# Kernel optimization log

Hardware: AMD Instinct MI355X
Metric: run time of the kernel (lower is better)

Reference implementation:

```python
import jax, jax.numpy as jnp
import numpy as np

B, L, D = 16, 2048, 192  # batch, frames_per_data, units
H, K = 4, 12             # num_heads, key_dim (hardcoded in build())
EPS = 1e-3               # keras LayerNormalization default epsilon


def layer_norm(x, g, b):
    m = jnp.mean(x, axis=-1, keepdims=True)
    v = jnp.mean(jnp.square(x - m), axis=-1, keepdims=True)
    return (x - m) * jax.lax.rsqrt(v + EPS) * g + b


def conv1d_valid(x, w, b):
    # x: [B,L,C], w: [3,Cin,Cout] -> [B,L-2,Cout]
    return jax.lax.conv_general_dilated(
        x, w, window_strides=(1,), padding='VALID',
        dimension_numbers=('NWC', 'WIO', 'NWC')) + b


def setup_inputs() -> dict:
    key = jax.random.key(0)
    ks = jax.random.split(key, 16)
    s = 0.05
    return {
        'x': jax.random.normal(ks[0], (B, L, D), jnp.float32),
        'ln1_g': jnp.ones((D,), jnp.float32),
        'ln1_b': jnp.zeros((D,), jnp.float32),
        'wq': jax.random.normal(ks[1], (D, H, K), jnp.float32) * s,
        'bq': jnp.zeros((H, K), jnp.float32),
        'wk': jax.random.normal(ks[2], (D, H, K), jnp.float32) * s,
        'bk': jnp.zeros((H, K), jnp.float32),
        'wv': jax.random.normal(ks[3], (D, H, K), jnp.float32) * s,
        'bv': jnp.zeros((H, K), jnp.float32),
        'wo': jax.random.normal(ks[4], (H, K, D), jnp.float32) * s,
        'bo': jnp.zeros((D,), jnp.float32),
        'ln2_g': jnp.ones((D,), jnp.float32),
        'ln2_b': jnp.zeros((D,), jnp.float32),
        'c1_w': jax.random.normal(ks[5], (3, D, D), jnp.float32) * s,
        'c1_b': jnp.zeros((D,), jnp.float32),
        'c2_w': jax.random.normal(ks[6], (3, D, D), jnp.float32) * s,
        'c2_b': jnp.zeros((D,), jnp.float32),
    }


def reference(x, ln1_g, ln1_b, wq, bq, wk, bk, wv, bv, wo, bo,
              ln2_g, ln2_b, c1_w, c1_b, c2_w, c2_b):
    # --- LN1 + causal MHA + residual (dropout = identity at inference) ---
    xn = layer_norm(x, ln1_g, ln1_b)
    q = jnp.einsum('bld,dhk->blhk', xn, wq) + bq
    k = jnp.einsum('bld,dhk->blhk', xn, wk) + bk
    v = jnp.einsum('bld,dhk->blhk', xn, wv) + bv
    scores = jnp.einsum('blhk,bmhk->bhlm', q, k) / jnp.sqrt(jnp.float32(K))
    causal = jnp.tril(jnp.ones((L, L), jnp.float32))  # tril(True) mask
    scores = scores + (1.0 - causal) * (-1e9)          # keras additive mask
    attn = jax.nn.softmax(scores, axis=-1)
    ctx = jnp.einsum('bhlm,bmhk->blhk', attn, v)
    mha = jnp.einsum('blhk,hkd->bld', ctx, wo) + bo
    x = x + mha
    # --- LN2 + positionwise Conv1D feedforward + residual ---
    xn = layer_norm(x, ln2_g, ln2_b)
    h = jax.nn.relu(conv1d_valid(xn, c1_w, c1_b))      # [B,L-2,D]
    h = jnp.pad(h, ((0, 0), (1, 1), (0, 0)))           # ZeroPadding1D(1,1)
    h = conv1d_valid(h, c2_w, c2_b)                    # [B,L-2,D]
    h = jnp.pad(h, ((0, 0), (1, 1), (0, 0)))
    return x + h
```

## Files before the change

### kernel.cpp

```cpp
#include <hip/hip_runtime.h>
#include <hip/hip_bf16.h>

#define L_ 2048
#define D_ 192
#define HK_ 48
#define EPS_ 1e-3f
#define SCALE_ 0.28867513459481287f
#define LOG2E_ 1.4426950408889634f

typedef __hip_bfloat16 bf16;
typedef _Float16 f16;
typedef __fp16 hf16x2 __attribute__((ext_vector_type(2)));
typedef _Float16 f16x4 __attribute__((ext_vector_type(4)));
typedef __bf16 bf16x4 __attribute__((ext_vector_type(4)));
typedef __bf16 bf16x8 __attribute__((ext_vector_type(8)));
typedef float  f32x4  __attribute__((ext_vector_type(4)));

__device__ __forceinline__ float b2f(bf16 x) { return __bfloat162float(x); }
__device__ __forceinline__ bf16 f2b(float x) { return __float2bfloat16(x); }

__global__ __launch_bounds__(256) void k_prep_all(
    const float* __restrict__ c1w, const float* __restrict__ c2w,
    const float* __restrict__ wq, const float* __restrict__ wk, const float* __restrict__ wv,
    const float* __restrict__ bq, const float* __restrict__ bk, const float* __restrict__ bv,
    const float* __restrict__ wo,
    bf16* __restrict__ wrep1, bf16* __restrict__ wrep2,
    bf16* __restrict__ wrepq, float* __restrict__ bias144, bf16* __restrict__ wrepo)
{
    const int i = blockIdx.x * 256 + threadIdx.x;
    if (i < 110592) {
        const int k = i / 192, n = i - k * 192;
        wrep1[((size_t)(k >> 5) * 192 + n) * 32 + (k & 31)] = f2b(c1w[i]);
    } else if (i < 221184) {
        const int j = i - 110592;
        const int k = j / 192, n = j - k * 192;
        wrep2[((size_t)(k >> 5) * 192 + n) * 32 + (k & 31)] = f2b(c2w[j]);
    } else if (i < 248832) {
        const int j = i - 221184;
        const int kb = j / 4608, rem = j % 4608;
        const int n = rem / 32, kk = rem % 32;
        const int k = kb * 32 + kk;
        float v;
        if (n < 48)       v = wq[k * HK_ + n] * (SCALE_ * LOG2E_);
        else if (n < 96)  v = wk[k * HK_ + (n - 48)];
        else              v = wv[k * HK_ + (n - 96)];
        wrepq[j] = f2b(v);
    } else if (i < 248976) {
        const int j = i - 248832;
        bias144[j] = (j < 48) ? bq[j] * (SCALE_ * LOG2E_)
                   : (j < 96) ? bk[j - 48] : bv[j - 96];
    } else if (i < 261264) {
        const int j = i - 248976;
        const int kb = j / 6144, rem = j % 6144;
        const int n = rem / 32, kk = rem % 32;
        const int k = kb * 32 + kk;
        wrepo[j] = f2b(k < 48 ? wo[k * D_ + n] : 0.f);
    }
}

__global__ __launch_bounds__(256, 4) void k_ln_qkv(
    const float* __restrict__ x, const float* __restrict__ g1, const float* __restrict__ b1,
    const bf16* __restrict__ wrep, const float* __restrict__ bias144,
    f16* __restrict__ qo, f16* __restrict__ ko, f16* __restrict__ vt)
{
    __shared__ bf16 xn[32 * 200];
    const int tid = threadIdx.x;
    const int wave = tid >> 6, lane = tid & 63;
    const int rowbase = blockIdx.x * 32;
    const int b = rowbase >> 11;
    const int lrow0 = rowbase & 2047;

    const float gg0 = g1[lane], gg1 = g1[lane + 64], gg2 = g1[lane + 128];
    const float bb0 = b1[lane], bb1 = b1[lane + 64], bb2 = b1[lane + 128];
    for (int i = 0; i < 8; ++i) {
        const int r = wave * 8 + i;
        const float* xp = x + (size_t)(rowbase + r) * D_;
        const float x0 = xp[lane];
        const float x1 = xp[lane + 64];
        const float x2 = xp[lane + 128];
        float s = x0 + x1 + x2;
        float q = x0 * x0 + x1 * x1 + x2 * x2;
        #pragma unroll
        for (int m = 1; m < 64; m <<= 1) {
            s += __shfl_xor(s, m, 64);
            q += __shfl_xor(q, m, 64);
        }
        const float mean = s * (1.0f / 192.0f);
        const float var  = q * (1.0f / 192.0f) - mean * mean;
        const float rs   = rsqrtf(var + EPS_);
        xn[r * 200 + lane]       = f2b((x0 - mean) * rs * gg0 + bb0);
        xn[r * 200 + lane + 64]  = f2b((x1 - mean) * rs * gg1 + bb1);
        xn[r * 200 + lane + 128] = f2b((x2 - mean) * rs * gg2 + bb2);
    }

    if (tid < 128) {
        const int h  = tid >> 5;
        const int vc = 12 + ((tid >> 3) & 3);
        const int p0 = lrow0 + (tid & 7) * 4;
        f16x4 vv;
        vv[0] = vv[1] = vv[2] = vv[3] = (vc == 12) ? (f16)1.0f : (f16)0.0f;
        *(f16x4*)(vt + ((size_t)(b * 4 + h) * 16 + vc) * 2048 + p0) = vv;
    }
    __syncthreads();

    const int l15 = lane & 15, q4 = lane >> 4;
    const int rt = wave >> 1, g = wave & 1;
    const int ntlim = 5 - g;
    f32x4 acc[5];
    #pragma unroll
    for (int nt = 0; nt < 5; ++nt) acc[nt] = (f32x4){0.f, 0.f, 0.f, 0.f};

    const bf16* xrow = xn + (rt * 16 + l15) * 200 + q4 * 8;
    #pragma unroll
    for (int kb = 0; kb < 6; ++kb) {
        const bf16x8 a = *(const bf16x8*)(xrow + kb * 32);
        const bf16* wp = wrep + ((size_t)kb * 144 + l15) * 32 + q4 * 8
                       + (size_t)(g * 5) * 16 * 32;
        #pragma unroll
        for (int nt = 0; nt < 5; ++nt) {
            if (nt < ntlim) {
                const bf16x8 bfr = *(const bf16x8*)(wp + (size_t)nt * 16 * 32);
                acc[nt] = __builtin_amdgcn_mfma_f32_16x16x32_bf16(a, bfr, acc[nt], 0, 0, 0);
            }
        }
    }

    const int lr0 = lrow0 + rt * 16 + q4 * 4;
    #pragma unroll
    for (int nt = 0; nt < 5; ++nt) {
        if (nt < ntlim) {
            const int ntg = g * 5 + nt;
            const int col = ntg * 16 + l15;
            const float bd = bias144[col];
            if (ntg < 3) {
                const int h2 = col / 12, c12 = col - h2 * 12;
                #pragma unroll
                for (int reg = 0; reg < 4; ++reg)
                    qo[((size_t)(b * 4 + h2) * 2048 + lr0 + reg) * 12 + c12] =
                        (f16)(acc[nt][reg] + bd);
            } else if (ntg < 6) {
                const int ck = col - 48;
                const int h2 = ck / 12, c12 = ck - h2 * 12;
                #pragma unroll
                for (int reg = 0; reg < 4; ++reg)
                    ko[((size_t)(b * 4 + h2) * 2048 + lr0 + reg) * 12 + c12] =
                        (f16)(acc[nt][reg] + bd);
            } else {
                const int vcol = col - 96;
                const int h = vcol / 12, c12 = vcol % 12;
                f16x4 vv;
                #pragma unroll
                for (int reg = 0; reg < 4; ++reg) vv[reg] = (f16)(acc[nt][reg] + bd);
                *(f16x4*)(vt + ((size_t)(b * 4 + h) * 16 + c12) * 2048 +
                          lrow0 + rt * 16 + q4 * 4) = vv;
            }
        }
    }
}

__global__ __launch_bounds__(256, 8) void k_attn_part(
    const f16* __restrict__ qh, const f16* __restrict__ kh, const f16* __restrict__ vt,
    bf16* __restrict__ part_o, float* __restrict__ part_l)
{
    const int tid = threadIdx.x;
    const int wv = tid >> 6, lane = tid & 63;
    const int quad = lane >> 4, l15 = lane & 15;
    const int bh = blockIdx.x / 36;
    int r = blockIdx.x % 36;
    int qt = 0;
    while (r >= qt + 1) { r -= qt + 1; ++qt; }
    const int ks = r;
    const size_t base  = (size_t)bh * 2048 * 12;
    const size_t vbase = ((size_t)bh * 16 + l15) * 2048;
    const int kbase = ks * 256;
    const int qbase = qt * 256 + wv * 64;
    const bool diag = (ks == qt);
    const int ktmax = diag ? 4 * (wv + 1) : 16;

    f16x4 Qf[4];
    #pragma unroll
    for (int s = 0; s < 4; ++s) {
        f16x4 v;
        if (quad < 3)
            v = *(const f16x4*)(qh + base + (size_t)(qbase + s * 16 + l15) * 12 + quad * 4);
        else { v[0] = (f16)LOG2E_; v[1] = 0; v[2] = 0; v[3] = 0; }
        Qf[s] = v;
    }

    f32x4 O[4];
    #pragma unroll
    for (int s = 0; s < 4; ++s) O[s] = (f32x4){0.f, 0.f, 0.f, 0.f};

    for (int g = 0; g < ktmax; g += 2) {
        f16x4 Kg[2], Vg[2];
        #pragma unroll
        for (int u = 0; u < 2; ++u) {
            const int kt = g + u;
            f16x4 kf;
            if (quad < 3)
                kf = *(const f16x4*)(kh + base + (size_t)(kbase + kt * 16 + l15) * 12 + quad * 4);
            else { kf[0] = (f16)-6.0f; kf[1] = 0; kf[2] = 0; kf[3] = 0; }
            Kg[u] = kf;
            Vg[u] = *(const f16x4*)(vt + vbase + kbase + kt * 16 + quad * 4);
        }
        #pragma unroll
        for (int u = 0; u < 2; ++u) {
            const int k0 = kbase + (g + u) * 16 + quad * 4;
            #pragma unroll
            for (int s = 0; s < 4; ++s) {
                f32x4 sc = (f32x4){0.f, 0.f, 0.f, 0.f};
                sc = __builtin_amdgcn_mfma_f32_16x16x16f16(Kg[u], Qf[s], sc, 0, 0, 0);
                float p0 = __builtin_amdgcn_exp2f(sc[0]);
                float p1 = __builtin_amdgcn_exp2f(sc[1]);
                float p2 = __builtin_amdgcn_exp2f(sc[2]);
                float p3 = __builtin_amdgcn_exp2f(sc[3]);
                if (diag) {
                    const int qg = qbase + s * 16 + l15;
                    p0 = (k0 + 0 <= qg) ? p0 : 0.f;
                    p1 = (k0 + 1 <= qg) ? p1 : 0.f;
                    p2 = (k0 + 2 <= qg) ? p2 : 0.f;
                    p3 = (k0 + 3 <= qg) ? p3 : 0.f;
                }
                const hf16x2 lo = __builtin_amdgcn_cvt_pkrtz(p0, p1);
                const hf16x2 hi = __builtin_amdgcn_cvt_pkrtz(p2, p3);
                f16x4 p;
                p[0] = (f16)lo[0]; p[1] = (f16)lo[1];
                p[2] = (f16)hi[0]; p[3] = (f16)hi[1];
                O[s] = __builtin_amdgcn_mfma_f32_16x16x16f16(p, Vg[u], O[s], 0, 0, 0);
            }
        }
    }

    const size_t pobase = (size_t)(bh * 8 + ks) * 2048;
    #pragma unroll
    for (int s = 0; s < 4; ++s) {
        const int q16 = qbase + s * 16;
        #pragma unroll
        for (int j = 0; j < 4; ++j) {
            const int qq = q16 + quad * 4 + j;
            if (l15 < 12)       part_o[(pobase + qq) * 12 + l15] = f2b(O[s][j]);
            else if (l15 == 12) part_l[pobase + qq] = O[s][j];
        }
    }
}

__global__ __launch_bounds__(256, 4) void k_proj_ln2(
    const float* __restrict__ x, const bf16* __restrict__ part_o,
    const float* __restrict__ part_l, const bf16* __restrict__ wrepo,
    const float* __restrict__ bo, const float* __restrict__ g2,
    const float* __restrict__ lb2, bf16* __restrict__ x2b,
    bf16* __restrict__ xn2b)
{
    __shared__ bf16 ct[32 * 72];
    __shared__ float linv[128];
    __shared__ float psum[4][4][4][2];
    const int tid = threadIdx.x;
    const int wave = tid >> 6, lane = tid & 63;
    const int rowbase = blockIdx.x * 32;
    const int b = rowbase >> 11, lrow = rowbase & 2047;
    const int ns = (lrow >> 8) + 1;

    {
        const int sub = tid >> 7, pair = tid & 127;
        const int rr = pair >> 2, h = pair & 3;
        const size_t sb = (size_t)(b * 4 + h) * 8 * 2048 + lrow + rr;
        float o[8] = {0.f, 0.f, 0.f, 0.f, 0.f, 0.f, 0.f, 0.f};
        float l = 0.f;
        if (sub == 0) {
            #pragma unroll
            for (int s = 0; s < 8; ++s) {
                if (s < ns) {
                    const bf16x8 v = *(const bf16x8*)(part_o + (sb + (size_t)s * 2048) * 12);
                    #pragma unroll
                    for (int i = 0; i < 8; ++i) o[i] += (float)v[i];
                }
            }
        } else {
            #pragma unroll
            for (int s = 0; s < 8; ++s) {
                if (s < ns) {
                    l += part_l[sb + (size_t)s * 2048];
                    const bf16x4 v = *(const bf16x4*)(part_o + (sb + (size_t)s * 2048) * 12 + 8);
                    #pragma unroll
                    for (int i = 0; i < 4; ++i) o[i] += (float)v[i];
                }
            }
            linv[pair] = 1.0f / l;
        }
        __syncthreads();
        const float inv = linv[pair];
        if (sub == 0) {
            bf16x4 w0, w1;
            #pragma unroll
            for (int i = 0; i < 4; ++i) {
                w0[i] = (__bf16)(o[i] * inv);
                w1[i] = (__bf16)(o[4 + i] * inv);
            }
            *(bf16x4*)(ct + rr * 72 + h * 12)     = w0;
            *(bf16x4*)(ct + rr * 72 + h * 12 + 4) = w1;
        } else {
            bf16x4 w, z;
            #pragma unroll
            for (int i = 0; i < 4; ++i) {
                w[i] = (__bf16)(o[i] * inv);
                z[i] = (__bf16)0.0f;
            }
            *(bf16x4*)(ct + rr * 72 + h * 12 + 8)  = w;
            *(bf16x4*)(ct + rr * 72 + 48 + h * 4)  = z;
        }
    }
    __syncthreads();

    const int l15 = lane & 15, q4 = lane >> 4;
    const int rt = wave >> 1, g = wave & 1;
    f32x4 acc[6];
    #pragma unroll
    for (int j = 0; j < 6; ++j) acc[j] = (f32x4){0.f, 0.f, 0.f, 0.f};
    const bf16* arow = ct + (rt * 16 + l15) * 72 + q4 * 8;
    #pragma unroll
    for (int kb = 0; kb < 2; ++kb) {
        const bf16x8 a = *(const bf16x8*)(arow + kb * 32);
        const bf16* wp = wrepo + ((size_t)kb * 192 + l15) * 32 + q4 * 8
                       + (size_t)(g * 6) * 16 * 32;
        #pragma unroll
        for (int j = 0; j < 6; ++j) {
            const bf16x8 bb = *(const bf16x8*)(wp + (size_t)j * 16 * 32);
            acc[j] = __builtin_amdgcn_mfma_f32_16x16x32_bf16(a, bb, acc[j], 0, 0, 0);
        }
    }

    const int rw0 = rowbase + rt * 16 + q4 * 4;
    float sum[4] = {0.f, 0.f, 0.f, 0.f}, ssum[4] = {0.f, 0.f, 0.f, 0.f};
    #pragma unroll
    for (int j = 0; j < 6; ++j) {
        const int col = (g * 6 + j) * 16 + l15;
        const float bod = bo[col];
        #pragma unroll
        for (int reg = 0; reg < 4; ++reg) {
            const float v = acc[j][reg] + bod + x[(size_t)(rw0 + reg) * D_ + col];
            acc[j][reg] = v;
            x2b[(size_t)(rw0 + reg) * D_ + col] = f2b(v);
            sum[reg] += v; ssum[reg] += v * v;
        }
    }
    #pragma unroll
    for (int m = 1; m <= 8; m <<= 1) {
        #pragma unroll
        for (int reg = 0; reg < 4; ++reg) {
            sum[reg]  += __shfl_xor(sum[reg], m, 64);
            ssum[reg] += __shfl_xor(ssum[reg], m, 64);
        }
    }
    if (l15 == 0) {
        #pragma unroll
        for (int reg = 0; reg < 4; ++reg) {
            psum[wave][q4][reg][0] = sum[reg];
            psum[wave][q4][reg][1] = ssum[reg];
        }
    }
    __syncthreads();
    float mean[4], rs[4];
    #pragma unroll
    for (int reg = 0; reg < 4; ++reg) {
        const float st = sum[reg]  + psum[wave ^ 1][q4][reg][0];
        const float qt2 = ssum[reg] + psum[wave ^ 1][q4][reg][1];
        mean[reg] = st * (1.0f / 192.0f);
        const float var = qt2 * (1.0f / 192.0f) - mean[reg] * mean[reg];
        rs[reg] = rsqrtf(var + EPS_);
    }
    #pragma unroll
    for (int j = 0; j < 6; ++j) {
        const int col = (g * 6 + j) * 16 + l15;
        const float gg = g2[col], bb2 = lb2[col];
        #pragma unroll
        for (int reg = 0; reg < 4; ++reg)
            xn2b[(size_t)(rw0 + reg) * D_ + col] =
                f2b((acc[j][reg] - mean[reg]) * rs[reg] * gg + bb2);
    }
}

#define INROWB 400
#define NIN    36
#define NH     34
#define HTOFF  (NIN * INROWB)
__global__ __launch_bounds__(256, 4) void k_conv_fused(
    const bf16* __restrict__ act, const bf16* __restrict__ w1,
    const float* __restrict__ b1c, const bf16* __restrict__ w2,
    const float* __restrict__ b2c, const bf16* __restrict__ x2b,
    float* __restrict__ outf)
{
    __shared__ __align__(16) char lds[NIN * INROWB + NH * INROWB];

    const int tid = threadIdx.x;
    const int wave = tid >> 6, lane = tid & 63;
    const int m16 = lane & 15, q = lane >> 4;
    const int rowbase = blockIdx.x * 32;
    const int lrow = rowbase & (L_ - 1);

    {
        const bf16* src0 = act + ((long long)rowbase - 2) * D_;
        bf16x8 v[4];
        int dst[4];
        #pragma unroll
        for (int i = 0; i < 4; ++i) {
            const int g = tid + i * 256;
            if (g < 864) {
                v[i] = *(const bf16x8*)(src0 + g * 8);
                const int row = (g * 2731) >> 16;
                dst[i] = row * INROWB + (g - row * 24) * 16;
            }
        }
        #pragma unroll
        for (int i = 0; i < 4; ++i) {
            const int g = tid + i * 256;
            if (g < 864) *(bf16x8*)(lds + dst[i]) = v[i];
        }
    }

    const int laneA = m16 * INROWB + q * 16;
    const int colw = wave * 48;
    float bd1[3], bd2[3];
    #pragma unroll
    for (int j = 0; j < 3; ++j) {
        bd1[j] = b1c[colw + j * 16 + m16];
        bd2[j] = b2c[colw + j * 16 + m16];
    }
    __syncthreads();

    f32x4 acc1[3][3];
    #pragma unroll
    for (int mt = 0; mt < 3; ++mt)
        #pragma unroll
        for (int j = 0; j < 3; ++j) acc1[mt][j] = (f32x4){0.f, 0.f, 0.f, 0.f};

    #define LOADB(w, kb, j) \
        (*(const bf16x8*)((w) + ((size_t)(kb) * 192 + m16) * 32 + q * 8 \
                          + (size_t)(wave * 3 + (j)) * 16 * 32))
    {
        bf16x8 bB[2][3];
        #pragma unroll
        for (int j = 0; j < 3; ++j) bB[0][j] = LOADB(w1, 0, j);
        #pragma unroll
        for (int kb = 0; kb < 18; ++kb) {
            if (kb + 1 < 18) {
                #pragma unroll
                for (int j = 0; j < 3; ++j) bB[(kb + 1) & 1][j] = LOADB(w1, kb + 1, j);
            }
            const int t = kb / 6, c6 = kb % 6;
            bf16x8 a[3];
            #pragma unroll
            for (int mt = 0; mt < 3; ++mt)
                a[mt] = *(const bf16x8*)(lds + laneA + (mt * 16 + t) * INROWB + c6 * 64);
            #pragma unroll
            for (int j = 0; j < 3; ++j)
                #pragma unroll
                for (int mt = 0; mt < 3; ++mt)
                    acc1[mt][j] = __builtin_amdgcn_mfma_f32_16x16x32_bf16(
                        a[mt], bB[kb & 1][j], acc1[mt][j], 0, 0, 0);
        }
    }

    #pragma unroll
    for (int mt = 0; mt < 3; ++mt)
        #pragma unroll
        for (int j = 0; j < 3; ++j)
            #pragma unroll
            for (int reg = 0; reg < 4; ++reg) {
                const int hr = mt * 16 + q * 4 + reg;
                if (hr < NH) {
                    const int hm = lrow + hr - 1;
                    float v = fmaxf(acc1[mt][j][reg] + bd1[j], 0.f);
                    if (hm == 0 || hm == L_ - 1) v = 0.f;
                    *(bf16*)(lds + HTOFF + hr * INROWB + (colw + j * 16 + m16) * 2) = f2b(v);
                }
            }

    float xr[3][2][4];
    #pragma unroll
    for (int j = 0; j < 3; ++j)
        #pragma unroll
        for (int mt = 0; mt < 2; ++mt)
            #pragma unroll
            for (int reg = 0; reg < 4; ++reg)
                xr[j][mt][reg] = b2f(x2b[(size_t)(rowbase + mt * 16 + q * 4 + reg) * D_
                                         + colw + j * 16 + m16]);
    __syncthreads();

    f32x4 acc2[2][3];
    #pragma unroll
    for (int mt = 0; mt < 2; ++mt)
        #pragma unroll
        for (int j = 0; j < 3; ++j) acc2[mt][j] = (f32x4){0.f, 0.f, 0.f, 0.f};
    {
        bf16x8 bB[2][3];
        #pragma unroll
        for (int j = 0; j < 3; ++j) bB[0][j] = LOADB(w2, 0, j);
        #pragma unroll
        for (int kb = 0; kb < 18; ++kb) {
            if (kb + 1 < 18) {
                #pragma unroll
                for (int j = 0; j < 3; ++j) bB[(kb + 1) & 1][j] = LOADB(w2, kb + 1, j);
            }
            const int t = kb / 6, c6 = kb % 6;
            bf16x8 a[2];
            #pragma unroll
            for (int mt = 0; mt < 2; ++mt)
                a[mt] = *(const bf16x8*)(lds + HTOFF + laneA + (mt * 16 + t) * INROWB + c6 * 64);
            #pragma unroll
            for (int j = 0; j < 3; ++j)
                #pragma unroll
                for (int mt = 0; mt < 2; ++mt)
                    acc2[mt][j] = __builtin_amdgcn_mfma_f32_16x16x32_bf16(
                        a[mt], bB[kb & 1][j], acc2[mt][j], 0, 0, 0);
        }
    }
    #undef LOADB

    #pragma unroll
    for (int j = 0; j < 3; ++j)
        #pragma unroll
        for (int mt = 0; mt < 2; ++mt)
            #pragma unroll
            for (int reg = 0; reg < 4; ++reg) {
                const int r = rowbase + mt * 16 + q * 4 + reg;
                const int m = r & (L_ - 1);
                float v = xr[j][mt][reg];
                if (m != 0 && m != L_ - 1) v += acc2[mt][j][reg] + bd2[j];
                outf[(size_t)r * D_ + colw + j * 16 + m16] = v;
            }
}

extern "C" void kernel_launch(void* const* d_in, const int* in_sizes, int n_in,
                              void* d_out, int out_size, void* d_ws, size_t ws_size,
                              hipStream_t stream)
{
    const float* x    = (const float*)d_in[0];
    const float* ln1g = (const float*)d_in[1];
    const float* ln1b = (const float*)d_in[2];
    const float* wq   = (const float*)d_in[3];
    const float* bq   = (const float*)d_in[4];
    const float* wk   = (const float*)d_in[5];
    const float* bk   = (const float*)d_in[6];
    const float* wv   = (const float*)d_in[7];
    const float* bv   = (const float*)d_in[8];
    const float* wo   = (const float*)d_in[9];
    const float* bo   = (const float*)d_in[10];
    const float* ln2g = (const float*)d_in[11];
    const float* ln2b = (const float*)d_in[12];
    const float* c1w  = (const float*)d_in[13];
    const float* c1b  = (const float*)d_in[14];
    const float* c2w  = (const float*)d_in[15];
    const float* c2b  = (const float*)d_in[16];

    const size_t ROWS = (size_t)16 * L_;
    char* ws = (char*)d_ws;
    size_t off = 4096;
    bf16* xn2b = (bf16*)(ws + off); off += ROWS * D_ * 2;
    off += 4096;
    bf16* hpb  = (bf16*)(ws + off); off += ROWS * D_ * 2;
    off += 4096;
    bf16* x2b  = (bf16*)(ws + off); off += ROWS * D_ * 2;
    f16* qb    = (f16*)(ws + off);   off += ROWS * HK_ * 2;
    f16* kb    = (f16*)(ws + off);   off += ROWS * HK_ * 2;
    f16* vt    = (f16*)(ws + off);   off += (size_t)64 * 16 * 2048 * 2;
    bf16* part_o = (bf16*)(ws + off); off += (size_t)64 * 8 * 2048 * 12 * 2;
    float* part_l = (float*)(ws + off); off += (size_t)64 * 8 * 2048 * 4;
    bf16* wrep1 = (bf16*)(ws + off); off += 576 * 192 * 2;
    bf16* wrep2 = (bf16*)(ws + off); off += 576 * 192 * 2;
    bf16* wrepq = (bf16*)(ws + off); off += 6 * 144 * 32 * 2;
    float* bias144 = (float*)(ws + off); off += 144 * 4;
    bf16* wrepo = (bf16*)(ws + off); off += 2 * 192 * 32 * 2;

    (void)hpb;
    k_prep_all   <<<1021, 256, 0, stream>>>(c1w, c2w, wq, wk, wv, bq, bk, bv, wo,
                                            wrep1, wrep2, wrepq, bias144, wrepo);
    k_ln_qkv     <<<1024, 256, 0, stream>>>(x, ln1g, ln1b, wrepq, bias144, qb, kb, vt);
    k_attn_part  <<<64 * 36, 256, 0, stream>>>(qb, kb, vt, part_o, part_l);
    k_proj_ln2   <<<1024, 256, 0, stream>>>(x, part_o, part_l, wrepo, bo, ln2g, ln2b,
                                            x2b, xn2b);
    k_conv_fused <<<1024, 256, 0, stream>>>(xn2b, wrep1, c1b, wrep2, c2b, x2b,
                                            (float*)d_out);
}
```

Baseline: 195.3 us.

## Fuse attention merge, output projection, LN2 and conv FFN into one kernel

```diff
diff --git a/kernel.cpp b/kernel.cpp
--- a/kernel.cpp
+++ b/kernel.cpp
@@ -244,189 +244,182 @@
     }
 }
 
-__global__ __launch_bounds__(256, 4) void k_proj_ln2(
+#define CIROWB 400
+#define R2OFF  14400
+#define X2OFF  28000
+#define PSOFF  40288
+__global__ __launch_bounds__(256, 3) void k_mega(
     const float* __restrict__ x, const bf16* __restrict__ part_o,
     const float* __restrict__ part_l, const bf16* __restrict__ wrepo,
     const float* __restrict__ bo, const float* __restrict__ g2,
-    const float* __restrict__ lb2, bf16* __restrict__ x2b,
-    bf16* __restrict__ xn2b)
+    const float* __restrict__ lb2, const bf16* __restrict__ w1,
+    const float* __restrict__ b1c, const bf16* __restrict__ w2,
+    const float* __restrict__ b2c, float* __restrict__ outf)
 {
-    __shared__ bf16 ct[32 * 72];
-    __shared__ float linv[128];
-    __shared__ float psum[4][4][4][2];
-    const int tid = threadIdx.x;
-    const int wave = tid >> 6, lane = tid & 63;
-    const int rowbase = blockIdx.x * 32;
-    const int b = rowbase >> 11, lrow = rowbase & 2047;
-    const int ns = (lrow >> 8) + 1;
-
-    {
-        const int sub = tid >> 7, pair = tid & 127;
-        const int rr = pair >> 2, h = pair & 3;
-        const size_t sb = (size_t)(b * 4 + h) * 8 * 2048 + lrow + rr;
-        float o[8] = {0.f, 0.f, 0.f, 0.f, 0.f, 0.f, 0.f, 0.f};
-        float l = 0.f;
-        if (sub == 0) {
-            #pragma unroll
-            for (int s = 0; s < 8; ++s) {
-                if (s < ns) {
-                    const bf16x8 v = *(const bf16x8*)(part_o + (sb + (size_t)s * 2048) * 12);
-                    #pragma unroll
-                    for (int i = 0; i < 8; ++i) o[i] += (float)v[i];
-                }
-            }
-        } else {
-            #pragma unroll
-            for (int s = 0; s < 8; ++s) {
-                if (s < ns) {
-                    l += part_l[sb + (size_t)s * 2048];
-                    const bf16x4 v = *(const bf16x4*)(part_o + (sb + (size_t)s * 2048) * 12 + 8);
-                    #pragma unroll
-                    for (int i = 0; i < 4; ++i) o[i] += (float)v[i];
-                }
-            }
-            linv[pair] = 1.0f / l;
-        }
-        __syncthreads();
-        const float inv = linv[pair];
-        if (sub == 0) {
-            bf16x4 w0, w1;
-            #pragma unroll
-            for (int i = 0; i < 4; ++i) {
-                w0[i] = (__bf16)(o[i] * inv);
-                w1[i] = (__bf16)(o[4 + i] * inv);
-            }
-            *(bf16x4*)(ct + rr * 72 + h * 12)     = w0;
-            *(bf16x4*)(ct + rr * 72 + h * 12 + 4) = w1;
-        } else {
-            bf16x4 w, z;
-            #pragma unroll
-            for (int i = 0; i < 4; ++i) {
-                w[i] = (__bf16)(o[i] * inv);
-                z[i] = (__bf16)0.0f;
-            }
-            *(bf16x4*)(ct + rr * 72 + h * 12 + 8)  = w;
-            *(bf16x4*)(ct + rr * 72 + 48 + h * 4)  = z;
-        }
-    }
-    __syncthreads();
-
-    const int l15 = lane & 15, q4 = lane >> 4;
-    const int rt = wave >> 1, g = wave & 1;
-    f32x4 acc[6];
-    #pragma unroll
-    for (int j = 0; j < 6; ++j) acc[j] = (f32x4){0.f, 0.f, 0.f, 0.f};
-    const bf16* arow = ct + (rt * 16 + l15) * 72 + q4 * 8;
-    #pragma unroll
-    for (int kb = 0; kb < 2; ++kb) {
-        const bf16x8 a = *(const bf16x8*)(arow + kb * 32);
-        const bf16* wp = wrepo + ((size_t)kb * 192 + l15) * 32 + q4 * 8
-                       + (size_t)(g * 6) * 16 * 32;
-        #pragma unroll
-        for (int j = 0; j < 6; ++j) {
-            const bf16x8 bb = *(const bf16x8*)(wp + (size_t)j * 16 * 32);
-            acc[j] = __builtin_amdgcn_mfma_f32_16x16x32_bf16(a, bb, acc[j], 0, 0, 0);
-        }
-    }
-
-    const int rw0 = rowbase + rt * 16 + q4 * 4;
-    float sum[4] = {0.f, 0.f, 0.f, 0.f}, ssum[4] = {0.f, 0.f, 0.f, 0.f};
-    #pragma unroll
-    for (int j = 0; j < 6; ++j) {
-        const int col = (g * 6 + j) * 16 + l15;
-        const float bod = bo[col];
-        #pragma unroll
-        for (int reg = 0; reg < 4; ++reg) {
-            const float v = acc[j][reg] + bod + x[(size_t)(rw0 + reg) * D_ + col];
-            acc[j][reg] = v;
-            x2b[(size_t)(rw0 + reg) * D_ + col] = f2b(v);
-            sum[reg] += v; ssum[reg] += v * v;
-        }
-    }
-    #pragma unroll
-    for (int m = 1; m <= 8; m <<= 1) {
-        #pragma unroll
-        for (int reg = 0; reg < 4; ++reg) {
-            sum[reg]  += __shfl_xor(sum[reg], m, 64);
-            ssum[reg] += __shfl_xor(ssum[reg], m, 64);
-        }
-    }
-    if (l15 == 0) {
-        #pragma unroll
-        for (int reg = 0; reg < 4; ++reg) {
-            psum[wave][q4][reg][0] = sum[reg];
-            psum[wave][q4][reg][1] = ssum[reg];
-        }
-    }
-    __syncthreads();
-    float mean[4], rs[4];
-    #pragma unroll
-    for (int reg = 0; reg < 4; ++reg) {
-        const float st = sum[reg]  + psum[wave ^ 1][q4][reg][0];
-        const float qt2 = ssum[reg] + psum[wave ^ 1][q4][reg][1];
-        mean[reg] = st * (1.0f / 192.0f);
-        const float var = qt2 * (1.0f / 192.0f) - mean[reg] * mean[reg];
-        rs[reg] = rsqrtf(var + EPS_);
-    }
-    #pragma unroll
-    for (int j = 0; j < 6; ++j) {
-        const int col = (g * 6 + j) * 16 + l15;
-        const float gg = g2[col], bb2 = lb2[col];
-        #pragma unroll
-        for (int reg = 0; reg < 4; ++reg)
-            xn2b[(size_t)(rw0 + reg) * D_ + col] =
-                f2b((acc[j][reg] - mean[reg]) * rs[reg] * gg + bb2);
-    }
-}
-
-#define INROWB 400
-#define NIN    36
-#define NH     34
-#define HTOFF  (NIN * INROWB)
-__global__ __launch_bounds__(256, 4) void k_conv_fused(
-    const bf16* __restrict__ act, const bf16* __restrict__ w1,
-    const float* __restrict__ b1c, const bf16* __restrict__ w2,
-    const float* __restrict__ b2c, const bf16* __restrict__ x2b,
-    float* __restrict__ outf)
-{
-    __shared__ __align__(16) char lds[NIN * INROWB + NH * INROWB];
+    __shared__ __align__(16) char lds[41824];
+    bf16* ct = (bf16*)(lds + R2OFF);
 
     const int tid = threadIdx.x;
     const int wave = tid >> 6, lane = tid & 63;
     const int m16 = lane & 15, q = lane >> 4;
     const int rowbase = blockIdx.x * 32;
-    const int lrow = rowbase & (L_ - 1);
-
+    const int b = rowbase >> 11, lrow = rowbase & 2047;
+    const int colw = wave * 48;
+
+    if (tid < 144) {
+        const int rr = tid >> 2, h = tid & 3;
+        int qrow = lrow + rr - 2;
+        qrow = qrow < 0 ? 0 : (qrow > 2047 ? 2047 : qrow);
+        const int nsq = (qrow >> 8) + 1;
+        const size_t sb = (size_t)(b * 4 + h) * 8 * 2048 + qrow;
+        float o[12];
+        #pragma unroll
+        for (int i = 0; i < 12; ++i) o[i] = 0.f;
+        float l = 0.f;
+        for (int s = 0; s < nsq; ++s) {
+            l += part_l[sb + (size_t)s * 2048];
+            const bf16x8 v8 = *(const bf16x8*)(part_o + (sb + (size_t)s * 2048) * 12);
+            const bf16x4 v4 = *(const bf16x4*)(part_o + (sb + (size_t)s * 2048) * 12 + 8);
+            #pragma unroll
+            for (int i = 0; i < 8; ++i) o[i] += (float)v8[i];
+            #pragma unroll
+            for (int i = 0; i < 4; ++i) o[8 + i] += (float)v4[i];
+        }
+        const float inv = 1.0f / l;
+        bf16* ctp = ct + rr * 72 + h * 12;
+        #pragma unroll
+        for (int i = 0; i < 12; ++i) ctp[i] = f2b(o[i] * inv);
+        bf16x4 z;
+        #pragma unroll
+        for (int i = 0; i < 4; ++i) z[i] = (__bf16)0.0f;
+        *(bf16x4*)(ct + rr * 72 + 48 + h * 4) = z;
+    } else {
+        const int idx = tid - 144;
+        if (idx < 108) {
+            bf16x8 z;
+            #pragma unroll
+            for (int i = 0; i < 8; ++i) z[i] = (__bf16)0.0f;
+            *(bf16x8*)(ct + 36 * 72 + idx * 8) = z;
+        }
+    }
+    float bd1[3], bd2[3], gg2[3], bbl2[3], bod[3];
+    #pragma unroll
+    for (int j = 0; j < 3; ++j) {
+        const int col = colw + j * 16 + m16;
+        bd1[j] = b1c[col]; bd2[j] = b2c[col];
+        gg2[j] = g2[col];  bbl2[j] = lb2[col]; bod[j] = bo[col];
+    }
+    __syncthreads();
+
+    f32x4 pv[3][3];
+    #pragma unroll
+    for (int mt = 0; mt < 3; ++mt)
+        #pragma unroll
+        for (int j = 0; j < 3; ++j) pv[mt][j] = (f32x4){0.f, 0.f, 0.f, 0.f};
+    #pragma unroll
+    for (int kb = 0; kb < 2; ++kb) {
+        bf16x8 a[3];
+        #pragma unroll
+        for (int mt = 0; mt < 3; ++mt)
+            a[mt] = *(const bf16x8*)(ct + (mt * 16 + m16) * 72 + kb * 32 + q * 8);
+        #pragma unroll
+        for (int j = 0; j < 3; ++j) {
+            const bf16x8 bb = *(const bf16x8*)(wrepo +
+                ((size_t)kb * 192 + (size_t)(wave * 3 + j) * 16 + m16) * 32 + q * 8);
+            #pragma unroll
+            for (int mt = 0; mt < 3; ++mt)
+                pv[mt][j] = __builtin_amdgcn_mfma_f32_16x16x32_bf16(a[mt], bb, pv[mt][j], 0, 0, 0);
+        }
+    }
+
+    #pragma unroll
+    for (int mt = 0; mt < 3; ++mt) {
+        const bool live = (mt < 2) || (q == 0);
+        #pragma unroll
+        for (int j = 0; j < 3; ++j) {
+            const int col = colw + j * 16 + m16;
+            #pragma unroll
+            for (int reg = 0; reg < 4; ++reg) {
+                int grow = lrow + mt * 16 + q * 4 + reg - 2;
+                grow = grow < 0 ? 0 : (grow > 2047 ? 2047 : grow);
+                float v = 0.f;
+                if (live)
+                    v = pv[mt][j][reg] + bod[j] + x[((size_t)b * 2048 + grow) * D_ + col];
+                pv[mt][j][reg] = v;
+            }
+        }
+    }
     {
-        const bf16* src0 = act + ((long long)rowbase - 2) * D_;
-        bf16x8 v[4];
-        int dst[4];
-        #pragma unroll
-        for (int i = 0; i < 4; ++i) {
-            const int g = tid + i * 256;
-            if (g < 864) {
-                v[i] = *(const bf16x8*)(src0 + g * 8);
-                const int row = (g * 2731) >> 16;
-                dst[i] = row * INROWB + (g - row * 24) * 16;
-            }
-        }
-        #pragma unroll
-        for (int i = 0; i < 4; ++i) {
-            const int g = tid + i * 256;
-            if (g < 864) *(bf16x8*)(lds + dst[i]) = v[i];
-        }
-    }
-
-    const int laneA = m16 * INROWB + q * 16;
-    const int colw = wave * 48;
-    float bd1[3], bd2[3];
-    #pragma unroll
-    for (int j = 0; j < 3; ++j) {
-        bd1[j] = b1c[colw + j * 16 + m16];
-        bd2[j] = b2c[colw + j * 16 + m16];
+        float* ps = (float*)(lds + PSOFF);
+        #pragma unroll
+        for (int mt = 0; mt < 3; ++mt) {
+            float sum[4], ssq[4];
+            #pragma unroll
+            for (int reg = 0; reg < 4; ++reg) {
+                sum[reg] = pv[mt][0][reg] + pv[mt][1][reg] + pv[mt][2][reg];
+                ssq[reg] = pv[mt][0][reg] * pv[mt][0][reg]
+                         + pv[mt][1][reg] * pv[mt][1][reg]
+                         + pv[mt][2][reg] * pv[mt][2][reg];
+            }
+            #pragma unroll
+            for (int m = 1; m <= 8; m <<= 1) {
+                #pragma unroll
+                for (int reg = 0; reg < 4; ++reg) {
+                    sum[reg] += __shfl_xor(sum[reg], m, 64);
+                    ssq[reg] += __shfl_xor(ssq[reg], m, 64);
+                }
+            }
+            if (m16 == 0) {
+                #pragma unroll
+                for (int reg = 0; reg < 4; ++reg) {
+                    const int tr = mt * 16 + q * 4 + reg;
+                    ps[(wave * 48 + tr) * 2 + 0] = sum[reg];
+                    ps[(wave * 48 + tr) * 2 + 1] = ssq[reg];
+                }
+            }
+        }
     }
     __syncthreads();
 
+    {
+        const float* ps = (const float*)(lds + PSOFF);
+        #pragma unroll
+        for (int mt = 0; mt < 3; ++mt) {
+            const bool live = (mt < 2) || (q == 0);
+            float mean[4], rs[4];
+            #pragma unroll
+            for (int reg = 0; reg < 4; ++reg) {
+                const int tr = mt * 16 + q * 4 + reg;
+                float st = 0.f, sq = 0.f;
+                #pragma unroll
+                for (int w = 0; w < 4; ++w) {
+                    st += ps[(w * 48 + tr) * 2 + 0];
+                    sq += ps[(w * 48 + tr) * 2 + 1];
+                }
+                mean[reg] = st * (1.0f / 192.0f);
+                const float var = sq * (1.0f / 192.0f) - mean[reg] * mean[reg];
+                rs[reg] = rsqrtf(var + EPS_);
+            }
+            if (live) {
+                #pragma unroll
+                for (int j = 0; j < 3; ++j) {
+                    const int col = colw + j * 16 + m16;
+                    #pragma unroll
+                    for (int reg = 0; reg < 4; ++reg) {
+                        const int tr = mt * 16 + q * 4 + reg;
+                        const float v = pv[mt][j][reg];
+                        const float xn = (v - mean[reg]) * rs[reg] * gg2[j] + bbl2[j];
+                        *(bf16*)(lds + tr * CIROWB + col * 2) = f2b(xn);
+                        if (tr >= 2 && tr < 34)
+                            *(bf16*)(lds + X2OFF + ((tr - 2) * 192 + col) * 2) = f2b(v);
+                    }
+                }
+            }
+        }
+    }
+    __syncthreads();
+
+    const int laneA = m16 * CIROWB + q * 16;
     f32x4 acc1[3][3];
     #pragma unroll
     for (int mt = 0; mt < 3; ++mt)
@@ -450,7 +443,7 @@
             bf16x8 a[3];
             #pragma unroll
             for (int mt = 0; mt < 3; ++mt)
-                a[mt] = *(const bf16x8*)(lds + laneA + (mt * 16 + t) * INROWB + c6 * 64);
+                a[mt] = *(const bf16x8*)(lds + laneA + (mt * 16 + t) * CIROWB + c6 * 64);
             #pragma unroll
             for (int j = 0; j < 3; ++j)
                 #pragma unroll
@@ -467,23 +460,13 @@
             #pragma unroll
             for (int reg = 0; reg < 4; ++reg) {
                 const int hr = mt * 16 + q * 4 + reg;
-                if (hr < NH) {
+                if (hr < 34) {
                     const int hm = lrow + hr - 1;
                     float v = fmaxf(acc1[mt][j][reg] + bd1[j], 0.f);
                     if (hm == 0 || hm == L_ - 1) v = 0.f;
-                    *(bf16*)(lds + HTOFF + hr * INROWB + (colw + j * 16 + m16) * 2) = f2b(v);
+                    *(bf16*)(lds + R2OFF + hr * CIROWB + (colw + j * 16 + m16) * 2) = f2b(v);
                 }
             }
-
-    float xr[3][2][4];
-    #pragma unroll
-    for (int j = 0; j < 3; ++j)
-        #pragma unroll
-        for (int mt = 0; mt < 2; ++mt)
-            #pragma unroll
-            for (int reg = 0; reg < 4; ++reg)
-                xr[j][mt][reg] = b2f(x2b[(size_t)(rowbase + mt * 16 + q * 4 + reg) * D_
-                                         + colw + j * 16 + m16]);
     __syncthreads();
 
     f32x4 acc2[2][3];
@@ -505,7 +488,7 @@
             bf16x8 a[2];
             #pragma unroll
             for (int mt = 0; mt < 2; ++mt)
-                a[mt] = *(const bf16x8*)(lds + HTOFF + laneA + (mt * 16 + t) * INROWB + c6 * 64);
+                a[mt] = *(const bf16x8*)(lds + R2OFF + laneA + (mt * 16 + t) * CIROWB + c6 * 64);
             #pragma unroll
             for (int j = 0; j < 3; ++j)
                 #pragma unroll
@@ -522,11 +505,13 @@
         for (int mt = 0; mt < 2; ++mt)
             #pragma unroll
             for (int reg = 0; reg < 4; ++reg) {
-                const int r = rowbase + mt * 16 + q * 4 + reg;
+                const int orr = mt * 16 + q * 4 + reg;
+                const int r = rowbase + orr;
                 const int m = r & (L_ - 1);
-                float v = xr[j][mt][reg];
+                const int col = colw + j * 16 + m16;
+                float v = b2f(*(const bf16*)(lds + X2OFF + (orr * 192 + col) * 2));
                 if (m != 0 && m != L_ - 1) v += acc2[mt][j][reg] + bd2[j];
-                outf[(size_t)r * D_ + colw + j * 16 + m16] = v;
+                outf[(size_t)r * D_ + col] = v;
             }
 }
 
@@ -554,12 +539,7 @@
 
     const size_t ROWS = (size_t)16 * L_;
     char* ws = (char*)d_ws;
-    size_t off = 4096;
-    bf16* xn2b = (bf16*)(ws + off); off += ROWS * D_ * 2;
-    off += 4096;
-    bf16* hpb  = (bf16*)(ws + off); off += ROWS * D_ * 2;
-    off += 4096;
-    bf16* x2b  = (bf16*)(ws + off); off += ROWS * D_ * 2;
+    size_t off = 0;
     f16* qb    = (f16*)(ws + off);   off += ROWS * HK_ * 2;
     f16* kb    = (f16*)(ws + off);   off += ROWS * HK_ * 2;
     f16* vt    = (f16*)(ws + off);   off += (size_t)64 * 16 * 2048 * 2;
@@ -571,13 +551,10 @@
     float* bias144 = (float*)(ws + off); off += 144 * 4;
     bf16* wrepo = (bf16*)(ws + off); off += 2 * 192 * 32 * 2;
 
-    (void)hpb;
-    k_prep_all   <<<1021, 256, 0, stream>>>(c1w, c2w, wq, wk, wv, bq, bk, bv, wo,
-                                            wrep1, wrep2, wrepq, bias144, wrepo);
-    k_ln_qkv     <<<1024, 256, 0, stream>>>(x, ln1g, ln1b, wrepq, bias144, qb, kb, vt);
-    k_attn_part  <<<64 * 36, 256, 0, stream>>>(qb, kb, vt, part_o, part_l);
-    k_proj_ln2   <<<1024, 256, 0, stream>>>(x, part_o, part_l, wrepo, bo, ln2g, ln2b,
-                                            x2b, xn2b);
-    k_conv_fused <<<1024, 256, 0, stream>>>(xn2b, wrep1, c1b, wrep2, c2b, x2b,
-                                            (float*)d_out);
+    k_prep_all  <<<1021, 256, 0, stream>>>(c1w, c2w, wq, wk, wv, bq, bk, bv, wo,
+                                           wrep1, wrep2, wrepq, bias144, wrepo);
+    k_ln_qkv    <<<1024, 256, 0, stream>>>(x, ln1g, ln1b, wrepq, bias144, qb, kb, vt);
+    k_attn_part <<<64 * 36, 256, 0, stream>>>(qb, kb, vt, part_o, part_l);
+    k_mega      <<<1024, 256, 0, stream>>>(x, part_o, part_l, wrepo, bo, ln2g, ln2b,
+                                           wrep1, c1b, wrep2, c2b, (float*)d_out);
 }
```

Result: no change. 193.1 us (-1.2%).
